# Optimization experiments

Hardware: AMD Instinct MI355X
Metric: run time of the kernel (lower is better)

Reference implementation:

```python
import jax, jax.numpy as jnp
import numpy as np

B, NX, NH, NY, K = 4096, 512, 512, 256, 8


def setup_inputs() -> dict:
    key = jax.random.key(0)
    k0, k1, k2, k3, k4, k5 = jax.random.split(key, 6)
    s = 1.0 / np.sqrt(NH)  # torch RNNCell init scale
    x = jax.random.normal(k0, (B, NX), jnp.float32)
    h = jax.random.normal(k1, (B, NH), jnp.float32)
    pi = jax.random.uniform(k2, (B, K), jnp.float32)
    pi = pi / pi.sum(axis=1, keepdims=True)  # __init_belief normalizes to sum 1
    W_ih = jax.random.uniform(k3, (K, NH, NX), jnp.float32, minval=-s, maxval=s)
    W_hh = jax.random.uniform(k4, (K, NH, NH), jnp.float32, minval=-s, maxval=s)
    W_out = jax.random.uniform(k5, (NY, NH), jnp.float32, minval=-s, maxval=s)
    return {"x": x, "h": h, "pi": pi, "W_ih": W_ih, "W_hh": W_hh, "W_out": W_out}


def reference(x, h, pi, W_ih, W_hh, W_out):
    # Per-state RNN cells (bias=False): h_k[:, :, k] = tanh(x @ W_ih[k].T + h @ W_hh[k].T)
    h_k = jnp.tanh(
        jnp.einsum('bx,knx->bnk', x, W_ih)
        + jnp.einsum('bh,knh->bnk', h, W_hh)
    )  # (B, NH, K)
    # out_k = out_layer applied per state: (B, NY, K)
    out_k = jnp.einsum('bnk,yn->byk', h_k, W_out)
    # belief-weighted soft combination of hidden states: states[b] = h_k[b] @ pi[b]
    h_mix = jnp.einsum('bnk,bk->bn', h_k, pi)  # (B, NH)
    out = h_mix @ W_out.T  # (B, NY)
    return (out, h_mix, out_k, h_k)
```

## Files before the change

kernel.cpp:

```cpp
#include <hip/hip_runtime.h>
#include <hip/hip_bf16.h>
#include <stdint.h>

typedef unsigned short u16;
typedef __attribute__((ext_vector_type(8))) short short8;
typedef __attribute__((ext_vector_type(4))) float f32x4;

#define BATCH 4096
#define OFF_OUT  0
#define OFF_HMIX (BATCH * 256)
#define OFF_OK   (OFF_HMIX + BATCH * 512)
#define OFF_HK   (OFF_OK + BATCH * 256 * 8)

#define WS_XB   0
#define WS_HB   (2097152)
#define WS_WIH  (4194304)
#define WS_WHH  (6291456)
#define WS_WOUT (8388608)
#define WS_T    (8519680)

__device__ __forceinline__ float b2f(u16 v) {
  union { uint32_t u; float f; } c; c.u = ((uint32_t)v) << 16; return c.f;
}
__device__ __forceinline__ u16 f2b(float f) {
  union { float f; uint32_t u; } c; c.f = f;
  uint32_t u = c.u;
  return (u16)((u + 0x7fffu + ((u >> 16) & 1u)) >> 16);
}

__device__ __forceinline__ void gload16(const u16* g, u16* l) {
  __builtin_amdgcn_global_load_lds(
      (const __attribute__((address_space(1))) void*)g,
      (__attribute__((address_space(3))) void*)l, 16, 0, 0);
}

__global__ __launch_bounds__(256) void k0_cvt(
    const float* __restrict__ x, const float* __restrict__ h,
    const float* __restrict__ Wih, const float* __restrict__ Whh,
    const float* __restrict__ Wout, u16* __restrict__ ws) {
  const int i = blockIdx.x * 256 + threadIdx.x;
  const float* src; int j; size_t dst;
  if      (i <  524288) { src = x;    j = i;           dst = WS_XB;   }
  else if (i < 1048576) { src = h;    j = i -  524288; dst = WS_HB;   }
  else if (i < 1572864) { src = Wih;  j = i - 1048576; dst = WS_WIH;  }
  else if (i < 2097152) { src = Whh;  j = i - 1572864; dst = WS_WHH;  }
  else                  { src = Wout; j = i - 2097152; dst = WS_WOUT; }
  const float4 v = ((const float4*)src)[j];
  ushort4 o;
  o.x = f2b(v.x); o.y = f2b(v.y); o.z = f2b(v.z); o.w = f2b(v.w);
  ((ushort4*)(ws + dst))[j] = o;
}

__global__ __launch_bounds__(256) void k1_gemm_tanh(
    const u16* __restrict__ xb, const u16* __restrict__ hb,
    const u16* __restrict__ Wih, const u16* __restrict__ Whh,
    u16* __restrict__ Tb) {
  __shared__ u16 As[128 * 64];
  __shared__ u16 Bs[128 * 64];
  const int tid  = threadIdx.x;
  const int lane = tid & 63;
  const int w    = tid >> 6;
  const int wm   = w >> 1, wn = w & 1;
  const int row0 = blockIdx.x * 128;
  const int col0 = blockIdx.y * 128;
  const int kk   = col0 >> 9;
  const int nh0  = col0 & 511;
  const int sr   = tid >> 3;
  const int sc   = ((tid & 7) ^ ((tid >> 3) & 7)) * 8;
  const int ldsw = (w * 8) * 64;

  const u16* WihK = Wih + (size_t)kk * 512 * 512;
  const u16* WhhK = Whh + (size_t)kk * 512 * 512;

  f32x4 acc[4][4] = {};

  for (int kt = 0; kt < 16; ++kt) {
    const int kb = kt * 64;
    const u16* Asrc; const u16* Bsrc; int ko;
    if (kb < 512) { Asrc = xb; Bsrc = WihK; ko = kb; }
    else          { Asrc = hb; Bsrc = WhhK; ko = kb - 512; }
#pragma unroll
    for (int ro = 0; ro < 4; ++ro) {
      gload16(Asrc + (size_t)(row0 + ro * 32 + sr) * 512 + ko + sc, &As[ro * 32 * 64 + ldsw]);
      gload16(Bsrc + (size_t)(nh0  + ro * 32 + sr) * 512 + ko + sc, &Bs[ro * 32 * 64 + ldsw]);
    }
    __syncthreads();
    const int l7 = lane & 7, quad = lane >> 4, rl = lane & 15;
#pragma unroll
    for (int ks = 0; ks < 2; ++ks) {
      short8 af[4], bf[4];
      const int cs = ((ks * 4 + quad) ^ l7) * 8;
#pragma unroll
      for (int i = 0; i < 4; ++i)
        af[i] = *(const short8*)&As[(wm * 64 + i * 16 + rl) * 64 + cs];
#pragma unroll
      for (int j = 0; j < 4; ++j)
        bf[j] = *(const short8*)&Bs[(wn * 64 + j * 16 + rl) * 64 + cs];
#pragma unroll
      for (int i = 0; i < 4; ++i)
#pragma unroll
        for (int j = 0; j < 4; ++j)
          acc[i][j] = __builtin_amdgcn_mfma_f32_16x16x32_bf16(af[i], bf[j], acc[i][j], 0, 0, 0);
    }
    __syncthreads();
  }

  const int quad = lane >> 4, cl = lane & 15;
#pragma unroll
  for (int i = 0; i < 4; ++i)
#pragma unroll
    for (int j = 0; j < 4; ++j)
#pragma unroll
      for (int r = 0; r < 4; ++r) {
        const int rr = row0 + wm * 64 + i * 16 + quad * 4 + r;
        const int cc = col0 + wn * 64 + j * 16 + cl;
        const float v = acc[i][j][r];
        const float e = __expf(2.0f * v);
        Tb[(size_t)rr * 4096 + cc] = f2b(1.0f - 2.0f / (e + 1.0f));
      }
}

__global__ __launch_bounds__(256) void k2_gemm_out(
    const u16* __restrict__ Tb, const u16* __restrict__ Wout,
    float* __restrict__ O) {
  __shared__ u16 As[128 * 64];
  __shared__ u16 Bs[128 * 64];
  const int tid  = threadIdx.x;
  const int lane = tid & 63;
  const int w    = tid >> 6;
  const int wm   = w >> 1, wn = w & 1;
  const int row0 = blockIdx.x * 128;
  const int y0   = blockIdx.y * 128;
  const int kk   = blockIdx.z;
  const int sr   = tid >> 3;
  const int sc   = ((tid & 7) ^ ((tid >> 3) & 7)) * 8;
  const int ldsw = (w * 8) * 64;

  f32x4 acc[4][4] = {};

  for (int kt = 0; kt < 8; ++kt) {
    const int kb = kt * 64;
#pragma unroll
    for (int ro = 0; ro < 4; ++ro) {
      gload16(Tb + (size_t)(row0 + ro * 32 + sr) * 4096 + kk * 512 + kb + sc,
              &As[ro * 32 * 64 + ldsw]);
      gload16(Wout + (size_t)(y0 + ro * 32 + sr) * 512 + kb + sc,
              &Bs[ro * 32 * 64 + ldsw]);
    }
    __syncthreads();
    const int l7 = lane & 7, quad = lane >> 4, rl = lane & 15;
#pragma unroll
    for (int ks = 0; ks < 2; ++ks) {
      short8 af[4], bf[4];
      const int cs = ((ks * 4 + quad) ^ l7) * 8;
#pragma unroll
      for (int i = 0; i < 4; ++i)
        af[i] = *(const short8*)&As[(wm * 64 + i * 16 + rl) * 64 + cs];
#pragma unroll
      for (int j = 0; j < 4; ++j)
        bf[j] = *(const short8*)&Bs[(wn * 64 + j * 16 + rl) * 64 + cs];
#pragma unroll
      for (int i = 0; i < 4; ++i)
#pragma unroll
        for (int j = 0; j < 4; ++j)
          acc[i][j] = __builtin_amdgcn_mfma_f32_16x16x32_bf16(af[i], bf[j], acc[i][j], 0, 0, 0);
    }
    __syncthreads();
  }

  const int quad = lane >> 4, cl = lane & 15;
#pragma unroll
  for (int i = 0; i < 4; ++i)
#pragma unroll
    for (int j = 0; j < 4; ++j)
#pragma unroll
      for (int r = 0; r < 4; ++r) {
        const int rr = row0 + wm * 64 + i * 16 + quad * 4 + r;
        const int cc = y0 + wn * 64 + j * 16 + cl;
        O[(size_t)rr * 2048 + kk * 256 + cc] = acc[i][j][r];
      }
}

__global__ __launch_bounds__(512) void k3_epi(const float* __restrict__ pi,
                                              const u16* __restrict__ Tb,
                                              float* __restrict__ dout) {
  const int b   = blockIdx.x;
  const int tid = threadIdx.x;
  float* O = dout + OFF_OK;

  float pif[8];
#pragma unroll
  for (int k = 0; k < 8; ++k) pif[k] = pi[b * 8 + k];

  float tv[8]; float hm = 0.0f;
#pragma unroll
  for (int k = 0; k < 8; ++k) {
    const float v = b2f(Tb[(size_t)b * 4096 + k * 512 + tid]);
    tv[k] = v; hm += pif[k] * v;
  }
  float ov[8]; float om = 0.0f;
  if (tid < 256) {
#pragma unroll
    for (int k = 0; k < 8; ++k) {
      const float v = O[(size_t)b * 2048 + k * 256 + tid];
      ov[k] = v; om += pif[k] * v;
    }
  }
  __syncthreads();

  float4* tw = (float4*)&dout[OFF_HK + (size_t)b * 4096 + tid * 8];
  tw[0] = make_float4(tv[0], tv[1], tv[2], tv[3]);
  tw[1] = make_float4(tv[4], tv[5], tv[6], tv[7]);
  dout[OFF_HMIX + (size_t)b * 512 + tid] = hm;

  if (tid < 256) {
    float4* ow = (float4*)&O[(size_t)b * 2048 + tid * 8];
    ow[0] = make_float4(ov[0], ov[1], ov[2], ov[3]);
    ow[1] = make_float4(ov[4], ov[5], ov[6], ov[7]);
    dout[OFF_OUT + (size_t)b * 256 + tid] = om;
  }
}

extern "C" void kernel_launch(void* const* d_in, const int* in_sizes, int n_in,
                              void* d_out, int out_size, void* d_ws, size_t ws_size,
                              hipStream_t stream) {
  const float* x    = (const float*)d_in[0];
  const float* h    = (const float*)d_in[1];
  const float* pi   = (const float*)d_in[2];
  const float* Wih  = (const float*)d_in[3];
  const float* Whh  = (const float*)d_in[4];
  const float* Wout = (const float*)d_in[5];
  float* out = (float*)d_out;
  u16* ws  = (u16*)d_ws;
  float* O = out + OFF_OK;

  k0_cvt<<<dim3(8320), 256, 0, stream>>>(x, h, Wih, Whh, Wout, ws);
  k1_gemm_tanh<<<dim3(32, 32), 256, 0, stream>>>(
      ws + WS_XB, ws + WS_HB, ws + WS_WIH, ws + WS_WHH, ws + WS_T);
  k2_gemm_out<<<dim3(32, 2, 8), 256, 0, stream>>>(ws + WS_T, ws + WS_WOUT, O);
  k3_epi<<<dim3(BATCH), 512, 0, stream>>>(pi, ws + WS_T, out);
}
```

Before: 226.7 us.

## Stage GEMM epilogues through LDS for vectorized stores; keep out_k intermediate in bf16

Both GEMM kernels now write their accumulator tiles into a padded LDS buffer, then emit coalesced 16-byte row stores instead of scattered 2-byte or 4-byte per-element writes. The out_k GEMM result is kept as a bf16 intermediate in the workspace rather than fp32 in the output buffer. This halves the intermediate traffic and lets the epilogue read a separate buffer and write out_k directly. The cost is extra LDS usage and a barrier per block, plus an added bf16 rounding on out_k and on the mixed output.

```diff
diff --git a/kernel.cpp b/kernel.cpp
--- a/kernel.cpp
+++ b/kernel.cpp
@@ -18,6 +18,7 @@
 #define WS_WHH  (6291456)
 #define WS_WOUT (8388608)
 #define WS_T    (8519680)
+#define WS_OB   (25296896)
 
 __device__ __forceinline__ float b2f(u16 v) {
   union { uint32_t u; float f; } c; c.u = ((uint32_t)v) << 16; return c.f;
@@ -55,8 +56,9 @@
     const u16* __restrict__ xb, const u16* __restrict__ hb,
     const u16* __restrict__ Wih, const u16* __restrict__ Whh,
     u16* __restrict__ Tb) {
-  __shared__ u16 As[128 * 64];
-  __shared__ u16 Bs[128 * 64];
+  __shared__ u16 S[128 * 136];
+  u16* As = S;
+  u16* Bs = S + 128 * 64;
   const int tid  = threadIdx.x;
   const int lane = tid & 63;
   const int w    = tid >> 6;
@@ -112,19 +114,29 @@
     for (int j = 0; j < 4; ++j)
 #pragma unroll
       for (int r = 0; r < 4; ++r) {
-        const int rr = row0 + wm * 64 + i * 16 + quad * 4 + r;
-        const int cc = col0 + wn * 64 + j * 16 + cl;
+        const int row = wm * 64 + i * 16 + quad * 4 + r;
+        const int col = wn * 64 + j * 16 + cl;
         const float v = acc[i][j][r];
         const float e = __expf(2.0f * v);
-        Tb[(size_t)rr * 4096 + cc] = f2b(1.0f - 2.0f / (e + 1.0f));
+        S[row * 136 + col] = f2b(1.0f - 2.0f / (e + 1.0f));
       }
+  __syncthreads();
+#pragma unroll
+  for (int it = 0; it < 8; ++it) {
+    const int idx = it * 256 + tid;
+    const int c = idx & 15;
+    const int r = idx >> 4;
+    *(short8*)&Tb[(size_t)(row0 + r) * 4096 + col0 + c * 8] =
+        *(const short8*)&S[r * 136 + c * 8];
+  }
 }
 
 __global__ __launch_bounds__(256) void k2_gemm_out(
     const u16* __restrict__ Tb, const u16* __restrict__ Wout,
-    float* __restrict__ O) {
-  __shared__ u16 As[128 * 64];
-  __shared__ u16 Bs[128 * 64];
+    u16* __restrict__ Ob) {
+  __shared__ u16 S[128 * 136];
+  u16* As = S;
+  u16* Bs = S + 128 * 64;
   const int tid  = threadIdx.x;
   const int lane = tid & 63;
   const int w    = tid >> 6;
@@ -175,18 +187,27 @@
     for (int j = 0; j < 4; ++j)
 #pragma unroll
       for (int r = 0; r < 4; ++r) {
-        const int rr = row0 + wm * 64 + i * 16 + quad * 4 + r;
-        const int cc = y0 + wn * 64 + j * 16 + cl;
-        O[(size_t)rr * 2048 + kk * 256 + cc] = acc[i][j][r];
+        const int row = wm * 64 + i * 16 + quad * 4 + r;
+        const int col = wn * 64 + j * 16 + cl;
+        S[row * 136 + col] = f2b(acc[i][j][r]);
       }
+  __syncthreads();
+#pragma unroll
+  for (int it = 0; it < 8; ++it) {
+    const int idx = it * 256 + tid;
+    const int c = idx & 15;
+    const int r = idx >> 4;
+    *(short8*)&Ob[(size_t)(row0 + r) * 2048 + kk * 256 + y0 + c * 8] =
+        *(const short8*)&S[r * 136 + c * 8];
+  }
 }
 
 __global__ __launch_bounds__(512) void k3_epi(const float* __restrict__ pi,
                                               const u16* __restrict__ Tb,
+                                              const u16* __restrict__ Ob,
                                               float* __restrict__ dout) {
   const int b   = blockIdx.x;
   const int tid = threadIdx.x;
-  float* O = dout + OFF_OK;
 
   float pif[8];
 #pragma unroll
@@ -198,23 +219,19 @@
     const float v = b2f(Tb[(size_t)b * 4096 + k * 512 + tid]);
     tv[k] = v; hm += pif[k] * v;
   }
-  float ov[8]; float om = 0.0f;
-  if (tid < 256) {
-#pragma unroll
-    for (int k = 0; k < 8; ++k) {
-      const float v = O[(size_t)b * 2048 + k * 256 + tid];
-      ov[k] = v; om += pif[k] * v;
-    }
-  }
-  __syncthreads();
-
   float4* tw = (float4*)&dout[OFF_HK + (size_t)b * 4096 + tid * 8];
   tw[0] = make_float4(tv[0], tv[1], tv[2], tv[3]);
   tw[1] = make_float4(tv[4], tv[5], tv[6], tv[7]);
   dout[OFF_HMIX + (size_t)b * 512 + tid] = hm;
 
   if (tid < 256) {
-    float4* ow = (float4*)&O[(size_t)b * 2048 + tid * 8];
+    float ov[8]; float om = 0.0f;
+#pragma unroll
+    for (int k = 0; k < 8; ++k) {
+      const float v = b2f(Ob[(size_t)b * 2048 + k * 256 + tid]);
+      ov[k] = v; om += pif[k] * v;
+    }
+    float4* ow = (float4*)&dout[OFF_OK + (size_t)b * 2048 + tid * 8];
     ow[0] = make_float4(ov[0], ov[1], ov[2], ov[3]);
     ow[1] = make_float4(ov[4], ov[5], ov[6], ov[7]);
     dout[OFF_OUT + (size_t)b * 256 + tid] = om;
@@ -232,11 +249,10 @@
   const float* Wout = (const float*)d_in[5];
   float* out = (float*)d_out;
   u16* ws  = (u16*)d_ws;
-  float* O = out + OFF_OK;
 
   k0_cvt<<<dim3(8320), 256, 0, stream>>>(x, h, Wih, Whh, Wout, ws);
   k1_gemm_tanh<<<dim3(32, 32), 256, 0, stream>>>(
       ws + WS_XB, ws + WS_HB, ws + WS_WIH, ws + WS_WHH, ws + WS_T);
-  k2_gemm_out<<<dim3(32, 2, 8), 256, 0, stream>>>(ws + WS_T, ws + WS_WOUT, O);
-  k3_epi<<<dim3(BATCH), 512, 0, stream>>>(pi, ws + WS_T, out);
-}
+  k2_gemm_out<<<dim3(32, 2, 8), 256, 0, stream>>>(ws + WS_T, ws + WS_WOUT, ws + WS_OB);
+  k3_epi<<<dim3(BATCH), 512, 0, stream>>>(pi, ws + WS_T, ws + WS_OB, out);
+}
```

New measurement: 220.6 us. 1.03x faster.
